# Kernel optimization log

Hardware: AMD Instinct MI355X
Metric: run time of the kernel (lower is better)

Reference implementation:

```python
import jax, jax.numpy as jnp
import numpy as np
from jax import lax

EPS = 1e-06
B, T, F = 32, 8192, 128


def setup_inputs() -> dict:
    key = jax.random.key(0)
    k1, k2 = jax.random.split(key)
    x = jax.random.uniform(k1, (B, T, F), dtype=jnp.float32)
    state = jax.random.uniform(k2, (B, 1, F), dtype=jnp.float32)
    log_s = jnp.log(jnp.full((F,), 0.025, dtype=jnp.float32))
    log_alpha = jnp.log(jnp.full((F,), 0.98, dtype=jnp.float32))
    log_delta = jnp.log(jnp.full((F,), 2.0, dtype=jnp.float32))
    log_r = jnp.log(jnp.full((F,), 0.5, dtype=jnp.float32))
    return {"x": x, "state": state, "log_s": log_s, "log_alpha": log_alpha,
            "log_delta": log_delta, "log_r": log_r}


def reference(x, state, log_s, log_alpha, log_delta, log_r):
    # per-channel gains, broadcast over (B, T, F)
    s = jnp.exp(log_s)          # (F,)
    alpha = jnp.exp(log_alpha)  # (F,)
    delta = jnp.exp(log_delta)  # (F,)
    r = jnp.exp(log_r)          # (F,)

    carry0 = state[:, 0, :]  # (B, F)

    def step(c, xt):
        c = (1.0 - s) * c + s * xt  # (B, F)
        return c, c

    # scan over time: xs are (T, B, F)
    final_state, E = lax.scan(step, carry0, jnp.swapaxes(x, 0, 1))
    E = jnp.swapaxes(E, 0, 1)  # (B, T, F)

    y = (x / (EPS + E) ** alpha + delta) ** r - delta ** r
    new_state = final_state[:, None, :]  # (B, 1, F)
    return y, new_state
```

## Files before the change

### kernel.cpp

```cpp
#include <hip/hip_runtime.h>
#include <math.h>

#define EPS 1e-6f

constexpr int B_ = 32;
constexpr int T_ = 8192;
constexpr int F_ = 128;
constexpr int FG = F_ / 4;
constexpr int FH = F_ / 2;

__device__ __forceinline__ float fpow(float b, float e) {
    return exp2f(e * __log2f(b));
}

template<int NC>
__global__ __launch_bounds__(256) void pcen_pass1(
    const float4* __restrict__ x4,
    const float*  __restrict__ log_s,
    float4* __restrict__ S4)
{
    constexpr int L = T_ / NC;
    const int fg    = threadIdx.x & 31;
    const int slot  = threadIdx.x >> 5;
    const int cb    = blockIdx.x % (NC / 8);
    const int b     = blockIdx.x / (NC / 8);
    const int chunk = cb * 8 + slot;

    const float4 lsv = reinterpret_cast<const float4*>(log_s)[fg];
    const float s0 = expf(lsv.x), s1 = expf(lsv.y), s2 = expf(lsv.z), s3 = expf(lsv.w);
    const float a0 = 1.f - s0,   a1 = 1.f - s1,    a2 = 1.f - s2,    a3 = 1.f - s3;

    const float4* xp = x4 + ((size_t)b * T_ + (size_t)chunk * L) * FG + fg;

    float c0 = 0.f, c1 = 0.f, c2 = 0.f, c3 = 0.f;
    #pragma unroll
    for (int i = 0; i < L; ++i) {
        const float4 xv = xp[(size_t)i * FG];
        c0 = fmaf(a0, c0, s0 * xv.x);
        c1 = fmaf(a1, c1, s1 * xv.y);
        c2 = fmaf(a2, c2, s2 * xv.z);
        c3 = fmaf(a3, c3, s3 * xv.w);
    }
    S4[((size_t)b * NC + chunk) * FG + fg] = make_float4(c0, c1, c2, c3);
}

template<int NC>
__global__ __launch_bounds__(32) void pcen_pass2(
    const float4* __restrict__ state4,
    const float*  __restrict__ log_s,
    const float4* __restrict__ S4,
    float4* __restrict__ carry4,
    float4* __restrict__ new_state4)
{
    constexpr int L = T_ / NC;
    const int fg = threadIdx.x;
    const int b  = blockIdx.x;

    const float4 lsv = reinterpret_cast<const float4*>(log_s)[fg];
    const float aL0 = fpow(1.f - expf(lsv.x), (float)L);
    const float aL1 = fpow(1.f - expf(lsv.y), (float)L);
    const float aL2 = fpow(1.f - expf(lsv.z), (float)L);
    const float aL3 = fpow(1.f - expf(lsv.w), (float)L);

    float4 c = state4[(size_t)b * FG + fg];
    #pragma unroll 8
    for (int k = 0; k < NC; ++k) {
        const size_t idx = ((size_t)b * NC + k) * FG + fg;
        carry4[idx] = c;
        const float4 Sv = S4[idx];
        c.x = fmaf(aL0, c.x, Sv.x);
        c.y = fmaf(aL1, c.y, Sv.y);
        c.z = fmaf(aL2, c.z, Sv.z);
        c.w = fmaf(aL3, c.w, Sv.w);
    }
    new_state4[(size_t)b * FG + fg] = c;
}

template<int NC>
__global__ __launch_bounds__(256) void pcen_pass3(
    const float2* __restrict__ x2,
    const float*  __restrict__ log_s,
    const float*  __restrict__ log_alpha,
    const float*  __restrict__ log_delta,
    const float*  __restrict__ log_r,
    const float2* __restrict__ carry2,
    float2* __restrict__ y2)
{
    constexpr int L = T_ / NC;
    const int lane  = threadIdx.x & 63;
    const int slot  = threadIdx.x >> 6;
    const int cb    = blockIdx.x % (NC / 4);
    const int b     = blockIdx.x / (NC / 4);
    const int chunk = cb * 4 + slot;

    const float2 lsv = reinterpret_cast<const float2*>(log_s)[lane];
    const float s0 = expf(lsv.x), s1 = expf(lsv.y);
    const float a0 = 1.f - s0,   a1 = 1.f - s1;

    const float2 lav = reinterpret_cast<const float2*>(log_alpha)[lane];
    const float2 ldv = reinterpret_cast<const float2*>(log_delta)[lane];
    const float2 lrv = reinterpret_cast<const float2*>(log_r)[lane];
    const float na0 = -expf(lav.x), na1 = -expf(lav.y);
    const float d0 = expf(ldv.x),  d1 = expf(ldv.y);
    const float r0 = expf(lrv.x),  r1 = expf(lrv.y);
    const float dr0 = fpow(d0, r0), dr1 = fpow(d1, r1);

    float2 c = carry2[((size_t)b * NC + chunk) * FH + lane];

    const size_t base = ((size_t)b * T_ + (size_t)chunk * L) * FH + lane;
    const float2* xp = x2 + base;
    float2*       yp = y2 + base;

    #pragma unroll
    for (int i = 0; i < L; i += 4) {
        float2 xv0 = xp[(size_t)(i + 0) * FH];
        float2 xv1 = xp[(size_t)(i + 1) * FH];
        float2 xv2 = xp[(size_t)(i + 2) * FH];
        float2 xv3 = xp[(size_t)(i + 3) * FH];

        float2 yv0, yv1, yv2, yv3;

        c.x = fmaf(a0, c.x, s0 * xv0.x);
        c.y = fmaf(a1, c.y, s1 * xv0.y);
        yv0.x = exp2f(r0 * __log2f(xv0.x * exp2f(na0 * __log2f(EPS + c.x)) + d0)) - dr0;
        yv0.y = exp2f(r1 * __log2f(xv0.y * exp2f(na1 * __log2f(EPS + c.y)) + d1)) - dr1;

        c.x = fmaf(a0, c.x, s0 * xv1.x);
        c.y = fmaf(a1, c.y, s1 * xv1.y);
        yv1.x = exp2f(r0 * __log2f(xv1.x * exp2f(na0 * __log2f(EPS + c.x)) + d0)) - dr0;
        yv1.y = exp2f(r1 * __log2f(xv1.y * exp2f(na1 * __log2f(EPS + c.y)) + d1)) - dr1;

        c.x = fmaf(a0, c.x, s0 * xv2.x);
        c.y = fmaf(a1, c.y, s1 * xv2.y);
        yv2.x = exp2f(r0 * __log2f(xv2.x * exp2f(na0 * __log2f(EPS + c.x)) + d0)) - dr0;
        yv2.y = exp2f(r1 * __log2f(xv2.y * exp2f(na1 * __log2f(EPS + c.y)) + d1)) - dr1;

        c.x = fmaf(a0, c.x, s0 * xv3.x);
        c.y = fmaf(a1, c.y, s1 * xv3.y);
        yv3.x = exp2f(r0 * __log2f(xv3.x * exp2f(na0 * __log2f(EPS + c.x)) + d0)) - dr0;
        yv3.y = exp2f(r1 * __log2f(xv3.y * exp2f(na1 * __log2f(EPS + c.y)) + d1)) - dr1;

        yp[(size_t)(i + 0) * FH] = yv0;
        yp[(size_t)(i + 1) * FH] = yv1;
        yp[(size_t)(i + 2) * FH] = yv2;
        yp[(size_t)(i + 3) * FH] = yv3;
    }
}

template<int NC>
static void launch_all(const float* x, const float* state,
                       const float* log_s, const float* log_alpha,
                       const float* log_delta, const float* log_r,
                       float* y, float* new_state, float* ws, hipStream_t stream)
{
    const float4* x4      = (const float4*)x;
    const float4* state4  = (const float4*)state;
    float4* new_state4    = (float4*)new_state;
    float4* S4            = (float4*)ws;
    float4* carry4        = S4 + (size_t)B_ * NC * FG;

    pcen_pass1<NC><<<dim3(B_ * (NC / 8)), dim3(256), 0, stream>>>(x4, log_s, S4);
    pcen_pass2<NC><<<dim3(B_), dim3(32), 0, stream>>>(state4, log_s, S4, carry4, new_state4);
    pcen_pass3<NC><<<dim3(B_ * (NC / 4)), dim3(256), 0, stream>>>(
        (const float2*)x, log_s, log_alpha, log_delta, log_r,
        (const float2*)carry4, (float2*)y);
}

extern "C" void kernel_launch(void* const* d_in, const int* in_sizes, int n_in,
                              void* d_out, int out_size, void* d_ws, size_t ws_size,
                              hipStream_t stream)
{
    const float* x         = (const float*)d_in[0];
    const float* state     = (const float*)d_in[1];
    const float* log_s     = (const float*)d_in[2];
    const float* log_alpha = (const float*)d_in[3];
    const float* log_delta = (const float*)d_in[4];
    const float* log_r     = (const float*)d_in[5];

    float* y         = (float*)d_out;
    float* new_state = y + (size_t)B_ * T_ * F_;

    const size_t need256 = 2ull * B_ * 256 * F_ * sizeof(float);
    const size_t need128 = 2ull * B_ * 128 * F_ * sizeof(float);
    if (ws_size >= need256) {
        launch_all<256>(x, state, log_s, log_alpha, log_delta, log_r,
                        y, new_state, (float*)d_ws, stream);
    } else if (ws_size >= need128) {
        launch_all<128>(x, state, log_s, log_alpha, log_delta, log_r,
                        y, new_state, (float*)d_ws, stream);
    } else {
        launch_all<64>(x, state, log_s, log_alpha, log_delta, log_r,
                       y, new_state, (float*)d_ws, stream);
    }
}
```

Baseline: 82.06 us.

## Fuse carry propagation into output pass via truncated decayed chunk-sum lookback

Removes the serial per-batch carry-propagation kernel. Each output block now reconstructs its starting carry by summing preceding chunk partial sums weighted by powers of the chunk decay factor. It stops early once the weights fall below a threshold, and the last chunk writes the new state. This eliminates one launch and a latency-bound serial pass at the cost of redundant lookback reads and a truncation approximation. The output expression also folds a multiply-add into an fma.

```diff
diff --git a/kernel.cpp b/kernel.cpp
--- a/kernel.cpp
+++ b/kernel.cpp
@@ -45,46 +45,16 @@
 }
 
 template<int NC>
-__global__ __launch_bounds__(32) void pcen_pass2(
-    const float4* __restrict__ state4,
-    const float*  __restrict__ log_s,
-    const float4* __restrict__ S4,
-    float4* __restrict__ carry4,
-    float4* __restrict__ new_state4)
-{
-    constexpr int L = T_ / NC;
-    const int fg = threadIdx.x;
-    const int b  = blockIdx.x;
-
-    const float4 lsv = reinterpret_cast<const float4*>(log_s)[fg];
-    const float aL0 = fpow(1.f - expf(lsv.x), (float)L);
-    const float aL1 = fpow(1.f - expf(lsv.y), (float)L);
-    const float aL2 = fpow(1.f - expf(lsv.z), (float)L);
-    const float aL3 = fpow(1.f - expf(lsv.w), (float)L);
-
-    float4 c = state4[(size_t)b * FG + fg];
-    #pragma unroll 8
-    for (int k = 0; k < NC; ++k) {
-        const size_t idx = ((size_t)b * NC + k) * FG + fg;
-        carry4[idx] = c;
-        const float4 Sv = S4[idx];
-        c.x = fmaf(aL0, c.x, Sv.x);
-        c.y = fmaf(aL1, c.y, Sv.y);
-        c.z = fmaf(aL2, c.z, Sv.z);
-        c.w = fmaf(aL3, c.w, Sv.w);
-    }
-    new_state4[(size_t)b * FG + fg] = c;
-}
-
-template<int NC>
 __global__ __launch_bounds__(256) void pcen_pass3(
     const float2* __restrict__ x2,
+    const float2* __restrict__ state2,
     const float*  __restrict__ log_s,
     const float*  __restrict__ log_alpha,
     const float*  __restrict__ log_delta,
     const float*  __restrict__ log_r,
-    const float2* __restrict__ carry2,
-    float2* __restrict__ y2)
+    const float2* __restrict__ S2,
+    float2* __restrict__ y2,
+    float2* __restrict__ ns2)
 {
     constexpr int L = T_ / NC;
     const int lane  = threadIdx.x & 63;
@@ -96,6 +66,27 @@
     const float2 lsv = reinterpret_cast<const float2*>(log_s)[lane];
     const float s0 = expf(lsv.x), s1 = expf(lsv.y);
     const float a0 = 1.f - s0,   a1 = 1.f - s1;
+    const float aL0 = fpow(a0, (float)L);
+    const float aL1 = fpow(a1, (float)L);
+
+    float c0 = 0.f, c1 = 0.f;
+    {
+        float coef0 = 1.f, coef1 = 1.f;
+        int k = chunk - 1;
+        for (; k >= 0; --k) {
+            if (coef0 < 1e-7f && coef1 < 1e-7f) break;
+            const float2 Sv = S2[((size_t)b * NC + k) * FH + lane];
+            c0 = fmaf(coef0, Sv.x, c0);
+            c1 = fmaf(coef1, Sv.y, c1);
+            coef0 *= aL0;
+            coef1 *= aL1;
+        }
+        if (k < 0) {
+            const float2 st = state2[(size_t)b * FH + lane];
+            c0 = fmaf(coef0, st.x, c0);
+            c1 = fmaf(coef1, st.y, c1);
+        }
+    }
 
     const float2 lav = reinterpret_cast<const float2*>(log_alpha)[lane];
     const float2 ldv = reinterpret_cast<const float2*>(log_delta)[lane];
@@ -105,11 +96,11 @@
     const float r0 = expf(lrv.x),  r1 = expf(lrv.y);
     const float dr0 = fpow(d0, r0), dr1 = fpow(d1, r1);
 
-    float2 c = carry2[((size_t)b * NC + chunk) * FH + lane];
-
     const size_t base = ((size_t)b * T_ + (size_t)chunk * L) * FH + lane;
     const float2* xp = x2 + base;
     float2*       yp = y2 + base;
+
+    float2 c; c.x = c0; c.y = c1;
 
     #pragma unroll
     for (int i = 0; i < L; i += 4) {
@@ -122,28 +113,32 @@
 
         c.x = fmaf(a0, c.x, s0 * xv0.x);
         c.y = fmaf(a1, c.y, s1 * xv0.y);
-        yv0.x = exp2f(r0 * __log2f(xv0.x * exp2f(na0 * __log2f(EPS + c.x)) + d0)) - dr0;
-        yv0.y = exp2f(r1 * __log2f(xv0.y * exp2f(na1 * __log2f(EPS + c.y)) + d1)) - dr1;
+        yv0.x = exp2f(r0 * __log2f(fmaf(xv0.x, exp2f(na0 * __log2f(EPS + c.x)), d0))) - dr0;
+        yv0.y = exp2f(r1 * __log2f(fmaf(xv0.y, exp2f(na1 * __log2f(EPS + c.y)), d1))) - dr1;
 
         c.x = fmaf(a0, c.x, s0 * xv1.x);
         c.y = fmaf(a1, c.y, s1 * xv1.y);
-        yv1.x = exp2f(r0 * __log2f(xv1.x * exp2f(na0 * __log2f(EPS + c.x)) + d0)) - dr0;
-        yv1.y = exp2f(r1 * __log2f(xv1.y * exp2f(na1 * __log2f(EPS + c.y)) + d1)) - dr1;
+        yv1.x = exp2f(r0 * __log2f(fmaf(xv1.x, exp2f(na0 * __log2f(EPS + c.x)), d0))) - dr0;
+        yv1.y = exp2f(r1 * __log2f(fmaf(xv1.y, exp2f(na1 * __log2f(EPS + c.y)), d1))) - dr1;
 
         c.x = fmaf(a0, c.x, s0 * xv2.x);
         c.y = fmaf(a1, c.y, s1 * xv2.y);
-        yv2.x = exp2f(r0 * __log2f(xv2.x * exp2f(na0 * __log2f(EPS + c.x)) + d0)) - dr0;
-        yv2.y = exp2f(r1 * __log2f(xv2.y * exp2f(na1 * __log2f(EPS + c.y)) + d1)) - dr1;
+        yv2.x = exp2f(r0 * __log2f(fmaf(xv2.x, exp2f(na0 * __log2f(EPS + c.x)), d0))) - dr0;
+        yv2.y = exp2f(r1 * __log2f(fmaf(xv2.y, exp2f(na1 * __log2f(EPS + c.y)), d1))) - dr1;
 
         c.x = fmaf(a0, c.x, s0 * xv3.x);
         c.y = fmaf(a1, c.y, s1 * xv3.y);
-        yv3.x = exp2f(r0 * __log2f(xv3.x * exp2f(na0 * __log2f(EPS + c.x)) + d0)) - dr0;
-        yv3.y = exp2f(r1 * __log2f(xv3.y * exp2f(na1 * __log2f(EPS + c.y)) + d1)) - dr1;
+        yv3.x = exp2f(r0 * __log2f(fmaf(xv3.x, exp2f(na0 * __log2f(EPS + c.x)), d0))) - dr0;
+        yv3.y = exp2f(r1 * __log2f(fmaf(xv3.y, exp2f(na1 * __log2f(EPS + c.y)), d1))) - dr1;
 
         yp[(size_t)(i + 0) * FH] = yv0;
         yp[(size_t)(i + 1) * FH] = yv1;
         yp[(size_t)(i + 2) * FH] = yv2;
         yp[(size_t)(i + 3) * FH] = yv3;
+    }
+
+    if (chunk == NC - 1) {
+        ns2[(size_t)b * FH + lane] = c;
     }
 }
 
@@ -153,17 +148,14 @@
                        const float* log_delta, const float* log_r,
                        float* y, float* new_state, float* ws, hipStream_t stream)
 {
-    const float4* x4      = (const float4*)x;
-    const float4* state4  = (const float4*)state;
-    float4* new_state4    = (float4*)new_state;
-    float4* S4            = (float4*)ws;
-    float4* carry4        = S4 + (size_t)B_ * NC * FG;
+    const float4* x4 = (const float4*)x;
+    float4* S4       = (float4*)ws;
 
     pcen_pass1<NC><<<dim3(B_ * (NC / 8)), dim3(256), 0, stream>>>(x4, log_s, S4);
-    pcen_pass2<NC><<<dim3(B_), dim3(32), 0, stream>>>(state4, log_s, S4, carry4, new_state4);
     pcen_pass3<NC><<<dim3(B_ * (NC / 4)), dim3(256), 0, stream>>>(
-        (const float2*)x, log_s, log_alpha, log_delta, log_r,
-        (const float2*)carry4, (float2*)y);
+        (const float2*)x, (const float2*)state,
+        log_s, log_alpha, log_delta, log_r,
+        (const float2*)S4, (float2*)y, (float2*)new_state);
 }
 
 extern "C" void kernel_launch(void* const* d_in, const int* in_sizes, int n_in,
@@ -180,8 +172,8 @@
     float* y         = (float*)d_out;
     float* new_state = y + (size_t)B_ * T_ * F_;
 
-    const size_t need256 = 2ull * B_ * 256 * F_ * sizeof(float);
-    const size_t need128 = 2ull * B_ * 128 * F_ * sizeof(float);
+    const size_t need256 = (size_t)B_ * 256 * F_ * sizeof(float);
+    const size_t need128 = (size_t)B_ * 128 * F_ * sizeof(float);
     if (ws_size >= need256) {
         launch_all<256>(x, state, log_s, log_alpha, log_delta, log_r,
                         y, new_state, (float*)d_ws, stream);
```

Result: faster. 75.41 us (-8.1%).
